# Performance work log

Hardware: AMD Instinct MI355X
Metric: run time of the kernel (lower is better)

The kernel has to match this reference:

```python
import jax, jax.numpy as jnp
from jax import lax
import numpy as np

B, DIM, H, W = 32, 256, 64, 64
HEADS = 4


def _dwconv(x, w, b, pad):
    # depthwise conv: w is (gc, 1, kh, kw), feature_group_count = gc
    y = lax.conv_general_dilated(x, w, window_strides=(1, 1), padding=pad,
                                 feature_group_count=w.shape[0])
    return y + b[None, :, None, None]


def setup_inputs() -> dict:
    key = jax.random.key(0)
    ks = jax.random.split(key, 9)
    gc = (DIM // 2) // 8  # branch_ratio = 0.125 -> 16
    s = 0.1
    return {
        "x": jax.random.normal(ks[0], (B, DIM, H, W), dtype=jnp.float32),
        "w_hw": jax.random.normal(ks[1], (gc, 1, 3, 3), dtype=jnp.float32) * s,
        "b_hw": jax.random.normal(ks[2], (gc,), dtype=jnp.float32) * s,
        "w_w": jax.random.normal(ks[3], (gc, 1, 1, 11), dtype=jnp.float32) * s,
        "b_w": jax.random.normal(ks[4], (gc,), dtype=jnp.float32) * s,
        "w_h": jax.random.normal(ks[5], (gc, 1, 11, 1), dtype=jnp.float32) * s,
        "b_h": jax.random.normal(ks[6], (gc,), dtype=jnp.float32) * s,
        "w_qkvl": jax.random.normal(ks[7], (DIM // 4 * HEADS, DIM // 2), dtype=jnp.float32) * s,
        "b_qkvl": jax.random.normal(ks[8], (DIM // 4 * HEADS,), dtype=jnp.float32) * s,
    }


def reference(x, w_hw, b_hw, w_w, b_w, w_h, b_h, w_qkvl, b_qkvl):
    Bx, C, Hx, Wx = x.shape
    C4 = C // 4
    gc = w_hw.shape[0]
    n_id = C // 2 - 3 * gc
    x1, x2 = jnp.split(x, 2, axis=1)  # each (B, C/2, H, W)

    # --- local branch: Inception depthwise conv + GELU ---
    xid = x1[:, :n_id]
    xhw = x1[:, n_id:n_id + gc]
    xw = x1[:, n_id + gc:n_id + 2 * gc]
    xh = x1[:, n_id + 2 * gc:]
    x1 = jnp.concatenate([
        xid,
        _dwconv(xhw, w_hw, b_hw, ((1, 1), (1, 1))),
        _dwconv(xw, w_w, b_w, ((0, 0), (5, 5))),
        _dwconv(xh, w_h, b_h, ((5, 5), (0, 0))),
    ], axis=1)
    x1 = jax.nn.gelu(x1, approximate=False)

    # --- global branch: 1x1 conv -> GELU -> pooled channel attention ---
    x2 = jnp.einsum('bchw,oc->bohw', x2, w_qkvl) + b_qkvl[None, :, None, None]
    x2 = jax.nn.gelu(x2, approximate=False)
    x2 = x2.reshape(Bx, HEADS, C4, Hx, Wx)

    q = jnp.sum(x2[:, :HEADS - 3], axis=1)          # (B, C4, H, W)
    k = x2[:, HEADS - 3]                             # (B, C4, H, W)
    v = x2[:, HEADS - 2].reshape(Bx, C4, Hx * Wx)    # (B, C4, HW)
    lfeat = x2[:, HEADS - 1]                         # (B, C4, H, W)

    # AvgPool2d(k=3, s=2, p=1) with count_include_pad=True (torch default)
    qp = lax.reduce_window(q, 0.0, lax.add, (1, 1, 3, 3), (1, 1, 2, 2),
                           ((0, 0), (0, 0), (1, 1), (1, 1))) / 9.0
    # MaxPool2d(k=2, s=2, p=0)
    kp = lax.reduce_window(k, -jnp.inf, lax.max, (1, 1, 2, 2), (1, 1, 2, 2), 'VALID')

    qf = qp.reshape(Bx, C4, -1)  # (B, C4, Np)
    kf = kp.reshape(Bx, C4, -1)  # (B, C4, Np)

    qk = jnp.einsum('bcn,bdn->bcd', qf, kf)          # (B, C4, C4)
    attn = jax.nn.softmax(qk, axis=1)                # softmax over dim=1, as in torch
    # torch: softmax(qk,1).transpose(1,2) @ v  ==  einsum over c
    out = jnp.einsum('bcd,bcm->bdm', attn, v).reshape(Bx, C4, Hx, Wx)

    return jnp.concatenate([x1, lfeat, out], axis=1)
```

## Files before the change

### kernel.cpp

```cpp
#include <hip/hip_runtime.h>
#include <hip/hip_bf16.h>

constexpr int kB   = 32;
constexpr int kC   = 256;
constexpr int kHW  = 4096;
constexpr int kC4  = 64;
constexpr int kGC  = 16;
constexpr int kNID = 80;

__device__ __forceinline__ float gelu_exact(float x) {
    return 0.5f * x * (1.0f + erff(x * 0.70710678118654752440f));
}

__device__ __forceinline__ float4 gelu4(float4 v) {
    return make_float4(gelu_exact(v.x), gelu_exact(v.y), gelu_exact(v.z), gelu_exact(v.w));
}

__global__ __launch_bounds__(256) void init_kernel(float4* __restrict__ qp)
{
    size_t i = (size_t)blockIdx.x * 256 + threadIdx.x;
    qp[i] = make_float4(0.f, 0.f, 0.f, 0.f);
}

__global__ __launch_bounds__(256) void part1_kernel(
    const float* __restrict__ x,
    const float* __restrict__ w_hw, const float* __restrict__ b_hw,
    const float* __restrict__ w_w,  const float* __restrict__ b_w,
    const float* __restrict__ w_h,  const float* __restrict__ b_h,
    float* __restrict__ out)
{
    int bc = blockIdx.x;
    int b  = bc >> 7;
    int c  = bc & 127;
    const float4* xp4 = (const float4*)(x   + (size_t)(b * kC + c) * kHW);
    float4*       op4 = (float4*)      (out + (size_t)(b * kC + c) * kHW);
    int tid = threadIdx.x;

    if (c < kNID) {
        for (int q = tid; q < 1024; q += 256)
            op4[q] = gelu4(xp4[q]);
    } else if (c < kNID + kGC) {
        int g = c - kNID;
        float wv[9];
        #pragma unroll
        for (int j = 0; j < 9; ++j) wv[j] = w_hw[g * 9 + j];
        float bias = b_hw[g];
        for (int q = tid; q < 1024; q += 256) {
            int h = q >> 4, wq = q & 15;
            float ax = bias, ay = bias, az = bias, aw = bias;
            #pragma unroll
            for (int dy = -1; dy <= 1; ++dy) {
                int rr = h + dy;
                if ((unsigned)rr >= 64u) continue;
                int base = rr * 16;
                float  l  = (wq > 0)  ? xp4[base + wq - 1].w : 0.f;
                float4 Bv = xp4[base + wq];
                float  r  = (wq < 15) ? xp4[base + wq + 1].x : 0.f;
                float w0 = wv[(dy + 1) * 3 + 0];
                float w1 = wv[(dy + 1) * 3 + 1];
                float w2 = wv[(dy + 1) * 3 + 2];
                ax += w0 * l    + w1 * Bv.x + w2 * Bv.y;
                ay += w0 * Bv.x + w1 * Bv.y + w2 * Bv.z;
                az += w0 * Bv.y + w1 * Bv.z + w2 * Bv.w;
                aw += w0 * Bv.z + w1 * Bv.w + w2 * r;
            }
            op4[q] = make_float4(gelu_exact(ax), gelu_exact(ay), gelu_exact(az), gelu_exact(aw));
        }
    } else if (c < kNID + 2 * kGC) {
        int g = c - (kNID + kGC);
        float wv[11];
        #pragma unroll
        for (int j = 0; j < 11; ++j) wv[j] = w_w[g * 11 + j];
        float bias = b_w[g];
        for (int q = tid; q < 1024; q += 256) {
            int h = q >> 4, wq = q & 15;
            int base = h * 16;
            float f[20];
            #pragma unroll
            for (int m = 0; m < 5; ++m) {
                int qq = wq + m - 2;
                float4 v;
                if ((unsigned)qq < 16u) v = xp4[base + qq];
                else                    v = make_float4(0.f, 0.f, 0.f, 0.f);
                f[4 * m + 0] = v.x; f[4 * m + 1] = v.y;
                f[4 * m + 2] = v.z; f[4 * m + 3] = v.w;
            }
            float a0 = bias, a1 = bias, a2 = bias, a3 = bias;
            #pragma unroll
            for (int m = 0; m < 11; ++m) {
                float w = wv[m];
                a0 += w * f[m + 3];
                a1 += w * f[m + 4];
                a2 += w * f[m + 5];
                a3 += w * f[m + 6];
            }
            op4[q] = make_float4(gelu_exact(a0), gelu_exact(a1), gelu_exact(a2), gelu_exact(a3));
        }
    } else {
        int g = c - (kNID + 2 * kGC);
        float wv[11];
        #pragma unroll
        for (int j = 0; j < 11; ++j) wv[j] = w_h[g * 11 + j];
        float bias = b_h[g];
        for (int q = tid; q < 1024; q += 256) {
            int h = q >> 4, wq = q & 15;
            float a0 = bias, a1 = bias, a2 = bias, a3 = bias;
            #pragma unroll
            for (int m = 0; m < 11; ++m) {
                int rr = h + m - 5;
                if ((unsigned)rr < 64u) {
                    float4 v = xp4[rr * 16 + wq];
                    float w = wv[m];
                    a0 += w * v.x; a1 += w * v.y; a2 += w * v.z; a3 += w * v.w;
                }
            }
            op4[q] = make_float4(gelu_exact(a0), gelu_exact(a1), gelu_exact(a2), gelu_exact(a3));
        }
    }
}

__global__ __launch_bounds__(256, 4) void conv1x1_kernel(
    const float* __restrict__ x,
    const float* __restrict__ w_qkvl, const float* __restrict__ b_qkvl,
    float* __restrict__ qp, float* __restrict__ kp,
    float* __restrict__ out)
{
    __shared__ float Ws[32][64];
    __shared__ float Xs[32 * 256];
    int pb   = blockIdx.x;
    int p0   = pb * 256;
    int head = blockIdx.y;
    int o0   = head * 64;
    int b    = blockIdx.z;
    int t    = threadIdx.x;
    int og   = t >> 5;
    int tp   = t & 31;

    float acc[8][8] = {};
    for (int kc = 0; kc < 4; ++kc) {
        #pragma unroll
        for (int r = 0; r < 2; ++r) {
            int g = t + r * 256;
            int o = g & 63, kq = g >> 6;
            float4 w4 = *(const float4*)&w_qkvl[(size_t)(o0 + o) * 128 + kc * 32 + kq * 4];
            Ws[kq * 4 + 0][o] = w4.x;
            Ws[kq * 4 + 1][o] = w4.y;
            Ws[kq * 4 + 2][o] = w4.z;
            Ws[kq * 4 + 3][o] = w4.w;
        }
        #pragma unroll
        for (int r = 0; r < 8; ++r) {
            int g = t + r * 256;
            int k = g >> 6, cch = g & 63;
            int cph = (cch >> 1) + (cch & 1) * 32;
            *(float4*)&Xs[k * 256 + cph * 4] =
                *(const float4*)&x[(size_t)(b * kC + 128 + kc * 32 + k) * kHW + p0 + cch * 4];
        }
        __syncthreads();
        for (int k = 0; k < 32; ++k) {
            const float* xrow = &Xs[k * 256];
            float4 wa = *(const float4*)&Ws[k][og * 8];
            float4 wb = *(const float4*)&Ws[k][og * 8 + 4];
            float4 xa = *(const float4*)&xrow[tp * 4];
            float4 xb = *(const float4*)&xrow[128 + tp * 4];
            float w8[8] = {wa.x, wa.y, wa.z, wa.w, wb.x, wb.y, wb.z, wb.w};
            float x8[8] = {xa.x, xa.y, xa.z, xa.w, xb.x, xb.y, xb.z, xb.w};
            #pragma unroll
            for (int i = 0; i < 8; ++i)
                #pragma unroll
                for (int j = 0; j < 8; ++j)
                    acc[i][j] += w8[i] * x8[j];
        }
        __syncthreads();
    }

    if (head < 2) {
        float* Ps = &Xs[0];
        int r  = tp >> 3;
        int m0 = (tp & 7) * 4;
        #pragma unroll
        for (int i = 0; i < 8; ++i) {
            int o = og * 8 + i;
            float bias = b_qkvl[o0 + o];
            float y[8];
            #pragma unroll
            for (int j = 0; j < 8; ++j) y[j] = gelu_exact(acc[i][j] + bias);
            float s[4];
            if (head == 0) {
                float left = __shfl_up(y[7], 1);
                if ((tp & 7) == 0) left = 0.0f;
                s[0] = left + y[0] + y[1];
                s[1] = y[1] + y[2] + y[3];
                s[2] = y[3] + y[4] + y[5];
                s[3] = y[5] + y[6] + y[7];
            } else {
                s[0] = fmaxf(y[0], y[1]);
                s[1] = fmaxf(y[2], y[3]);
                s[2] = fmaxf(y[4], y[5]);
                s[3] = fmaxf(y[6], y[7]);
            }
            *(float4*)&Ps[o * 128 + r * 32 + m0] = *(float4*)s;
        }
        __syncthreads();
        if (head == 0) {
            bool last = (pb == 15);
            for (int e = t; e < 2048; e += 256) {
                int o = e >> 5, m = e & 31;
                const float* P = &Ps[o * 128 + m];
                float pv0 = P[0], pv1 = P[32], pv2 = P[64], pv3 = P[96];
                float* dst = &qp[(((size_t)(b * kC4 + o)) << 10) + (2 * pb) * 32 + m];
                dst[32] = (pv1 + pv2 + pv3) * (1.0f / 9.0f);
                atomicAdd(dst, (pv0 + pv1) * (1.0f / 9.0f));
                if (!last) atomicAdd(dst + 64, pv3 * (1.0f / 9.0f));
            }
        } else {
            for (int e = t; e < 2048; e += 256) {
                int o = e >> 5, m = e & 31;
                const float* P = &Ps[o * 128 + m];
                float* dst = &kp[(((size_t)(b * kC4 + o)) << 10) + (2 * pb) * 32 + m];
                dst[0]  = fmaxf(P[0],  P[32]);
                dst[32] = fmaxf(P[64], P[96]);
            }
        }
    } else {
        int cbase = (head == 2) ? 192 : 128;
        #pragma unroll
        for (int i = 0; i < 8; ++i) {
            int o = og * 8 + i;
            float bias = b_qkvl[o0 + o];
            float4 ya = make_float4(gelu_exact(acc[i][0] + bias), gelu_exact(acc[i][1] + bias),
                                    gelu_exact(acc[i][2] + bias), gelu_exact(acc[i][3] + bias));
            float4 yb = make_float4(gelu_exact(acc[i][4] + bias), gelu_exact(acc[i][5] + bias),
                                    gelu_exact(acc[i][6] + bias), gelu_exact(acc[i][7] + bias));
            float* dst = &out[(size_t)(b * kC + cbase + o) * kHW + p0 + tp * 8];
            *(float4*)dst       = ya;
            *(float4*)(dst + 4) = yb;
        }
    }
}

__global__ __launch_bounds__(256) void qk_softmax_kernel(
    const float* __restrict__ qp, const float* __restrict__ kp,
    float* __restrict__ attn)
{
    __shared__ float qs[64][132];
    __shared__ float ksT[128][20];
    __shared__ float qk_s[64][17];
    __shared__ float mx[16], sm[16];
    int dt = blockIdx.x;
    int b  = blockIdx.y;
    int t  = threadIdx.x;
    int c  = t & 63, dg = t >> 6;

    float acc[4] = {};
    for (int nc = 0; nc < 8; ++nc) {
        #pragma unroll
        for (int r = 0; r < 8; ++r) {
            int g = t + r * 256;
            int cc = g >> 5, n4 = g & 31;
            *(float4*)&qs[cc][n4 * 4] =
                *(const float4*)&qp[(size_t)(b * 64 + cc) * 1024 + nc * 128 + n4 * 4];
        }
        #pragma unroll
        for (int r = 0; r < 8; ++r) {
            int g = t + r * 256;
            int dl = g >> 7, n = g & 127;
            ksT[n][dl] = kp[(size_t)(b * 64 + dt * 16 + dl) * 1024 + nc * 128 + n];
        }
        __syncthreads();
        for (int n4 = 0; n4 < 32; ++n4) {
            float4 qv = *(const float4*)&qs[c][n4 * 4];
            float4 k0 = *(const float4*)&ksT[n4 * 4 + 0][dg * 4];
            float4 k1 = *(const float4*)&ksT[n4 * 4 + 1][dg * 4];
            float4 k2 = *(const float4*)&ksT[n4 * 4 + 2][dg * 4];
            float4 k3 = *(const float4*)&ksT[n4 * 4 + 3][dg * 4];
            acc[0] += qv.x * k0.x + qv.y * k1.x + qv.z * k2.x + qv.w * k3.x;
            acc[1] += qv.x * k0.y + qv.y * k1.y + qv.z * k2.y + qv.w * k3.y;
            acc[2] += qv.x * k0.z + qv.y * k1.z + qv.z * k2.z + qv.w * k3.z;
            acc[3] += qv.x * k0.w + qv.y * k1.w + qv.z * k2.w + qv.w * k3.w;
        }
        __syncthreads();
    }
    #pragma unroll
    for (int j = 0; j < 4; ++j) qk_s[c][dg * 4 + j] = acc[j];
    __syncthreads();
    if (t < 16) {
        float m = -1e30f;
        for (int cc = 0; cc < 64; ++cc) m = fmaxf(m, qk_s[cc][t]);
        float s = 0.f;
        for (int cc = 0; cc < 64; ++cc) s += expf(qk_s[cc][t] - m);
        mx[t] = m;
        sm[t] = 1.0f / s;
    }
    __syncthreads();
    #pragma unroll
    for (int j = 0; j < 4; ++j) {
        int d = dg * 4 + j;
        attn[(size_t)(b * 64 + c) * 64 + dt * 16 + d] = expf(acc[j] - mx[d]) * sm[d];
    }
}

__global__ __launch_bounds__(256) void out2_kernel(
    const float* __restrict__ attn, float* __restrict__ out)
{
    __shared__ float at[64][64];
    int b = blockIdx.y;
    int t = threadIdx.x;
    #pragma unroll
    for (int r = 0; r < 4; ++r) {
        int g = t + r * 256;
        *(float4*)&at[g >> 4][(g & 15) * 4] = *(const float4*)&attn[(size_t)b * 4096 + g * 4];
    }
    __syncthreads();
    int m = blockIdx.x * 256 + t;
    float* vcol = out + (size_t)(b * kC + 192) * kHW + m;
    float acc[64] = {};
    for (int c8 = 0; c8 < 8; ++c8) {
        float v[8];
        #pragma unroll
        for (int j = 0; j < 8; ++j) v[j] = vcol[(size_t)(c8 * 8 + j) * kHW];
        #pragma unroll
        for (int j = 0; j < 8; ++j) {
            float vv = v[j];
            const float* arow = &at[c8 * 8 + j][0];
            #pragma unroll
            for (int d4 = 0; d4 < 16; ++d4) {
                float4 a = *(const float4*)&arow[d4 * 4];
                acc[d4 * 4 + 0] += a.x * vv;
                acc[d4 * 4 + 1] += a.y * vv;
                acc[d4 * 4 + 2] += a.z * vv;
                acc[d4 * 4 + 3] += a.w * vv;
            }
        }
    }
    #pragma unroll
    for (int d = 0; d < 64; ++d)
        vcol[(size_t)d * kHW] = acc[d];
}

extern "C" void kernel_launch(void* const* d_in, const int* in_sizes, int n_in,
                              void* d_out, int out_size, void* d_ws, size_t ws_size,
                              hipStream_t stream)
{
    const float* x      = (const float*)d_in[0];
    const float* w_hw   = (const float*)d_in[1];
    const float* b_hw   = (const float*)d_in[2];
    const float* w_w    = (const float*)d_in[3];
    const float* b_w    = (const float*)d_in[4];
    const float* w_h    = (const float*)d_in[5];
    const float* b_h    = (const float*)d_in[6];
    const float* w_qkvl = (const float*)d_in[7];
    const float* b_qkvl = (const float*)d_in[8];
    float* out = (float*)d_out;

    char* w = (char*)d_ws;
    float* qp   = (float*)w;  w += (size_t)kB * kC4 * 1024 * 4;
    float* kp   = (float*)w;  w += (size_t)kB * kC4 * 1024 * 4;
    float* attn = (float*)w;  w += (size_t)kB * kC4 * kC4 * 4;

    init_kernel<<<dim3(2048), 256, 0, stream>>>((float4*)qp);
    part1_kernel<<<dim3(kB * 128), 256, 0, stream>>>(x, w_hw, b_hw, w_w, b_w, w_h, b_h, out);
    conv1x1_kernel<<<dim3(16, 4, kB), 256, 0, stream>>>(x, w_qkvl, b_qkvl, qp, kp, out);
    qk_softmax_kernel<<<dim3(4, kB), 256, 0, stream>>>(qp, kp, attn);
    out2_kernel<<<dim3(16, kB), 256, 0, stream>>>(attn, out);
}
```

Measured before the change: 484.7 us.

## Split QK reduction over spatial chunks with atomics and separate softmax kernel

Replaces the single qk_softmax kernel, which used only 128 blocks each looping over all 1024 pooled positions, with a split-K kernel. Each of 256 blocks computes a partial 64x64 QK tile over 128 positions and accumulates it into a zeroed workspace with atomicAdd. A new softmax kernel then normalizes that buffer. This adds one launch, a larger init and atomic traffic, and also changes the conv1x1 launch bounds occupancy hint and adds an unroll pragma.

```diff
diff --git a/kernel.cpp b/kernel.cpp
--- a/kernel.cpp
+++ b/kernel.cpp
@@ -16,10 +16,16 @@
     return make_float4(gelu_exact(v.x), gelu_exact(v.y), gelu_exact(v.z), gelu_exact(v.w));
 }
 
-__global__ __launch_bounds__(256) void init_kernel(float4* __restrict__ qp)
-{
-    size_t i = (size_t)blockIdx.x * 256 + threadIdx.x;
-    qp[i] = make_float4(0.f, 0.f, 0.f, 0.f);
+__global__ __launch_bounds__(256) void init_kernel(float4* __restrict__ qp, float4* __restrict__ qkb)
+{
+    int bid = blockIdx.x;
+    if (bid < 2048) {
+        size_t i = (size_t)bid * 256 + threadIdx.x;
+        qp[i] = make_float4(0.f, 0.f, 0.f, 0.f);
+    } else {
+        size_t i = (size_t)(bid - 2048) * 256 + threadIdx.x;
+        qkb[i] = make_float4(0.f, 0.f, 0.f, 0.f);
+    }
 }
 
 __global__ __launch_bounds__(256) void part1_kernel(
@@ -119,7 +125,7 @@
     }
 }
 
-__global__ __launch_bounds__(256, 4) void conv1x1_kernel(
+__global__ __launch_bounds__(256, 3) void conv1x1_kernel(
     const float* __restrict__ x,
     const float* __restrict__ w_qkvl, const float* __restrict__ b_qkvl,
     float* __restrict__ qp, float* __restrict__ kp,
@@ -157,6 +163,7 @@
                 *(const float4*)&x[(size_t)(b * kC + 128 + kc * 32 + k) * kHW + p0 + cch * 4];
         }
         __syncthreads();
+        #pragma unroll 2
         for (int k = 0; k < 32; ++k) {
             const float* xrow = &Xs[k * 256];
             float4 wa = *(const float4*)&Ws[k][og * 8];
@@ -239,64 +246,84 @@
     }
 }
 
-__global__ __launch_bounds__(256) void qk_softmax_kernel(
+__global__ __launch_bounds__(256) void qk_partial_kernel(
     const float* __restrict__ qp, const float* __restrict__ kp,
-    float* __restrict__ attn)
-{
-    __shared__ float qs[64][132];
-    __shared__ float ksT[128][20];
-    __shared__ float qk_s[64][17];
-    __shared__ float mx[16], sm[16];
-    int dt = blockIdx.x;
+    float* __restrict__ qkb)
+{
+    __shared__ float qsT[128][65];
+    __shared__ float ksT[128][65];
+    int nb = blockIdx.x;
     int b  = blockIdx.y;
     int t  = threadIdx.x;
-    int c  = t & 63, dg = t >> 6;
-
-    float acc[4] = {};
-    for (int nc = 0; nc < 8; ++nc) {
-        #pragma unroll
-        for (int r = 0; r < 8; ++r) {
-            int g = t + r * 256;
-            int cc = g >> 5, n4 = g & 31;
-            *(float4*)&qs[cc][n4 * 4] =
-                *(const float4*)&qp[(size_t)(b * 64 + cc) * 1024 + nc * 128 + n4 * 4];
-        }
-        #pragma unroll
-        for (int r = 0; r < 8; ++r) {
-            int g = t + r * 256;
-            int dl = g >> 7, n = g & 127;
-            ksT[n][dl] = kp[(size_t)(b * 64 + dt * 16 + dl) * 1024 + nc * 128 + n];
-        }
-        __syncthreads();
-        for (int n4 = 0; n4 < 32; ++n4) {
-            float4 qv = *(const float4*)&qs[c][n4 * 4];
-            float4 k0 = *(const float4*)&ksT[n4 * 4 + 0][dg * 4];
-            float4 k1 = *(const float4*)&ksT[n4 * 4 + 1][dg * 4];
-            float4 k2 = *(const float4*)&ksT[n4 * 4 + 2][dg * 4];
-            float4 k3 = *(const float4*)&ksT[n4 * 4 + 3][dg * 4];
-            acc[0] += qv.x * k0.x + qv.y * k1.x + qv.z * k2.x + qv.w * k3.x;
-            acc[1] += qv.x * k0.y + qv.y * k1.y + qv.z * k2.y + qv.w * k3.y;
-            acc[2] += qv.x * k0.z + qv.y * k1.z + qv.z * k2.z + qv.w * k3.z;
-            acc[3] += qv.x * k0.w + qv.y * k1.w + qv.z * k2.w + qv.w * k3.w;
-        }
-        __syncthreads();
-    }
-    #pragma unroll
-    for (int j = 0; j < 4; ++j) qk_s[c][dg * 4 + j] = acc[j];
+    int tc = t & 15;
+    int td = t >> 4;
+
+    #pragma unroll
+    for (int r = 0; r < 8; ++r) {
+        int g = t + r * 256;
+        int ch = g >> 5, n4 = g & 31;
+        float4 q4 = *(const float4*)&qp[(size_t)(b * 64 + ch) * 1024 + nb * 128 + n4 * 4];
+        qsT[n4 * 4 + 0][ch] = q4.x;
+        qsT[n4 * 4 + 1][ch] = q4.y;
+        qsT[n4 * 4 + 2][ch] = q4.z;
+        qsT[n4 * 4 + 3][ch] = q4.w;
+        float4 k4 = *(const float4*)&kp[(size_t)(b * 64 + ch) * 1024 + nb * 128 + n4 * 4];
+        ksT[n4 * 4 + 0][ch] = k4.x;
+        ksT[n4 * 4 + 1][ch] = k4.y;
+        ksT[n4 * 4 + 2][ch] = k4.z;
+        ksT[n4 * 4 + 3][ch] = k4.w;
+    }
     __syncthreads();
-    if (t < 16) {
+
+    float acc[4][4] = {};
+    #pragma unroll 4
+    for (int n = 0; n < 128; ++n) {
+        float4 q4 = *(const float4*)&qsT[n][tc * 4];
+        float4 k4 = *(const float4*)&ksT[n][td * 4];
+        float qa[4] = {q4.x, q4.y, q4.z, q4.w};
+        float ka[4] = {k4.x, k4.y, k4.z, k4.w};
+        #pragma unroll
+        for (int i = 0; i < 4; ++i)
+            #pragma unroll
+            for (int j = 0; j < 4; ++j)
+                acc[i][j] += qa[i] * ka[j];
+    }
+    #pragma unroll
+    for (int i = 0; i < 4; ++i)
+        #pragma unroll
+        for (int j = 0; j < 4; ++j)
+            atomicAdd(&qkb[((size_t)b * 64 + tc * 4 + i) * 64 + td * 4 + j], acc[i][j]);
+}
+
+__global__ __launch_bounds__(256) void softmax_kernel(
+    const float* __restrict__ qkb, float* __restrict__ attn)
+{
+    __shared__ float qk_s[64][65];
+    __shared__ float mxs[64], sms[64];
+    int b = blockIdx.x;
+    int t = threadIdx.x;
+    #pragma unroll
+    for (int r = 0; r < 16; ++r) {
+        int g = t + r * 256;
+        qk_s[g >> 6][g & 63] = qkb[(size_t)b * 4096 + g];
+    }
+    __syncthreads();
+    if (t < 64) {
         float m = -1e30f;
+        #pragma unroll 4
         for (int cc = 0; cc < 64; ++cc) m = fmaxf(m, qk_s[cc][t]);
         float s = 0.f;
+        #pragma unroll 4
         for (int cc = 0; cc < 64; ++cc) s += expf(qk_s[cc][t] - m);
-        mx[t] = m;
-        sm[t] = 1.0f / s;
+        mxs[t] = m;
+        sms[t] = 1.0f / s;
     }
     __syncthreads();
     #pragma unroll
-    for (int j = 0; j < 4; ++j) {
-        int d = dg * 4 + j;
-        attn[(size_t)(b * 64 + c) * 64 + dt * 16 + d] = expf(acc[j] - mx[d]) * sm[d];
+    for (int r = 0; r < 16; ++r) {
+        int g = t + r * 256;
+        int c = g >> 6, d = g & 63;
+        attn[(size_t)b * 4096 + g] = expf(qk_s[c][d] - mxs[d]) * sms[d];
     }
 }
 
@@ -357,10 +384,12 @@
     float* qp   = (float*)w;  w += (size_t)kB * kC4 * 1024 * 4;
     float* kp   = (float*)w;  w += (size_t)kB * kC4 * 1024 * 4;
     float* attn = (float*)w;  w += (size_t)kB * kC4 * kC4 * 4;
-
-    init_kernel<<<dim3(2048), 256, 0, stream>>>((float4*)qp);
+    float* qkb  = (float*)w;  w += (size_t)kB * kC4 * kC4 * 4;
+
+    init_kernel<<<dim3(2176), 256, 0, stream>>>((float4*)qp, (float4*)qkb);
     part1_kernel<<<dim3(kB * 128), 256, 0, stream>>>(x, w_hw, b_hw, w_w, b_w, w_h, b_h, out);
     conv1x1_kernel<<<dim3(16, 4, kB), 256, 0, stream>>>(x, w_qkvl, b_qkvl, qp, kp, out);
-    qk_softmax_kernel<<<dim3(4, kB), 256, 0, stream>>>(qp, kp, attn);
+    qk_partial_kernel<<<dim3(8, kB), 256, 0, stream>>>(qp, kp, qkb);
+    softmax_kernel<<<dim3(kB), 256, 0, stream>>>(qkb, attn);
     out2_kernel<<<dim3(16, kB), 256, 0, stream>>>(attn, out);
 }
```

Measured after the change: 451.8 us. 1.07x faster.
